# Kernel optimization log

Measured on AMD Instinct MI355X. Metric: run time of the kernel, lower is better.

## Reference

```python
import jax, jax.numpy as jnp
import numpy as np

N_NODES = 50000
N_EDGES = 500000
D_FEAT = 128
HIDDEN = 128
EPS = 1e-8


def _lin_init(key, fan_in, fan_out):
    return jax.random.normal(key, (fan_in, fan_out), dtype=jnp.float32) / np.sqrt(fan_in)


def setup_inputs() -> dict:
    key = jax.random.key(0)
    ks = jax.random.split(key, 16)
    h = jax.random.normal(ks[0], (N_NODES, D_FEAT), dtype=jnp.float32)
    coord = jax.random.normal(ks[1], (N_NODES, 3), dtype=jnp.float32)
    vel = jax.random.normal(ks[2], (N_NODES, 3), dtype=jnp.float32)
    edge_index = jax.random.randint(ks[3], (2, N_EDGES), 0, N_NODES, dtype=jnp.int32)
    return {
        "h": h, "coord": coord, "vel": vel, "edge_index": edge_index,
        "W_e1": _lin_init(ks[4], 2 * D_FEAT + 1, HIDDEN), "b_e1": jnp.zeros((HIDDEN,), jnp.float32),
        "W_e2": _lin_init(ks[5], HIDDEN, D_FEAT), "b_e2": jnp.zeros((D_FEAT,), jnp.float32),
        "W_c1": _lin_init(ks[6], D_FEAT, HIDDEN), "b_c1": jnp.zeros((HIDDEN,), jnp.float32),
        "W_c2": _lin_init(ks[7], HIDDEN, 1), "b_c2": jnp.zeros((1,), jnp.float32),
        "W_v1": _lin_init(ks[8], D_FEAT, HIDDEN), "b_v1": jnp.zeros((HIDDEN,), jnp.float32),
        "W_v2": _lin_init(ks[9], HIDDEN, 1), "b_v2": jnp.zeros((1,), jnp.float32),
        "W_n1": _lin_init(ks[10], 2 * D_FEAT, HIDDEN), "b_n1": jnp.zeros((HIDDEN,), jnp.float32),
        "W_n2": _lin_init(ks[11], HIDDEN, D_FEAT), "b_n2": jnp.zeros((D_FEAT,), jnp.float32),
    }


def reference(h, coord, vel, edge_index,
              W_e1, b_e1, W_e2, b_e2,
              W_c1, b_c1, W_c2, b_c2,
              W_v1, b_v1, W_v2, b_v2,
              W_n1, b_n1, W_n2, b_n2):
    act = jax.nn.silu
    r, c = edge_index[0], edge_index[1]
    n = coord.shape[0]

    # coord2radial with normalize=True
    diff = coord[r] - coord[c]                      # [E, 3]
    rad = jnp.sum(diff * diff, axis=-1, keepdims=True)  # [E, 1]
    norm = jnp.sqrt(jax.lax.stop_gradient(rad)) + EPS
    diff = diff / norm

    # edge_op: Linear -> act -> Linear -> act
    edge_in = jnp.concatenate([h[r], h[c], rad], axis=1)  # [E, 2D+1]
    m_ij = act(act(edge_in @ W_e1 + b_e1) @ W_e2 + b_e2)  # [E, D]

    # coord_op: Linear -> act -> Linear (scalar weight per edge)
    weights = act(m_ij @ W_c1 + b_c1) @ W_c2 + b_c2       # [E, 1]
    coors_sum = jax.ops.segment_sum(diff * weights, r, num_segments=n)  # [N, 3]

    # vel_op: Linear -> act -> Linear (scalar per node)
    vel_weights = act(h @ W_v1 + b_v1) @ W_v2 + b_v2      # [N, 1]
    coord_out = coord + coors_sum + vel * vel_weights

    # node aggregation + node_op: Linear -> act -> Linear
    m_i = jax.ops.segment_sum(m_ij, r, num_segments=h.shape[0])  # [N, D]
    agg = jnp.concatenate([h, m_i], axis=1)               # [N, 2D]
    h_out = act(agg @ W_n1 + b_n1) @ W_n2 + b_n2          # [N, D]
    return (h_out, coord_out)
```

## Files before the change

kernel.cpp:

```cpp
#include <hip/hip_runtime.h>
#include <stdint.h>

#define NN 50000
#define NE 500000
#define BLK 256
#define NEB ((NE + 127) / 128)
#define SST 136

#define BARRIER() asm volatile("s_waitcnt lgkmcnt(0)\n\ts_barrier" ::: "memory")

typedef __attribute__((ext_vector_type(8))) short bf16x8;
typedef __attribute__((ext_vector_type(4))) float f32x4;

__device__ __forceinline__ float silu(float x) { return x / (1.0f + __expf(-x)); }
__device__ __forceinline__ float bf2f(unsigned short s) {
    union { unsigned int u; float f; } v; v.u = ((unsigned int)s) << 16; return v.f;
}
__device__ __forceinline__ unsigned short f2bf(float f) {
    union { float f; unsigned int u; } v; v.f = f;
    return (unsigned short)((v.u + 0x7fffu + ((v.u >> 16) & 1u)) >> 16);
}
__device__ __forceinline__ unsigned int pack2(float a, float b) {
    return (unsigned int)f2bf(a) | ((unsigned int)f2bf(b) << 16);
}
__device__ __forceinline__ bf16x8 packf8(const float* p) {
    float4 f0 = *(const float4*)p; float4 f1 = *(const float4*)(p + 4);
    union { bf16x8 v; unsigned int u[4]; } o;
    o.u[0] = pack2(f0.x, f0.y); o.u[1] = pack2(f0.z, f0.w);
    o.u[2] = pack2(f1.x, f1.y); o.u[3] = pack2(f1.z, f1.w);
    return o.v;
}

__global__ void prep_h(const float* __restrict__ h, unsigned short* __restrict__ hb) {
    int i = blockIdx.x * 256 + threadIdx.x;
    if (i < NN * 128 / 4) {
        float4 v = ((const float4*)h)[i];
        uint2 o; o.x = pack2(v.x, v.y); o.y = pack2(v.z, v.w);
        ((uint2*)hb)[i] = o;
    }
}

__global__ void prep_w(const float* __restrict__ We1, const float* __restrict__ We2,
                       const float* __restrict__ Wc1, const float* __restrict__ Wv1,
                       const float* __restrict__ Wn1, const float* __restrict__ Wn2,
                       unsigned short* __restrict__ Wt1, unsigned short* __restrict__ Wt2,
                       unsigned short* __restrict__ Wt3, unsigned short* __restrict__ Wv1t,
                       unsigned short* __restrict__ Wn1t, unsigned short* __restrict__ Wn2t) {
    int i = blockIdx.x * 256 + threadIdx.x;
    if (i < 32768) {
        int j = i >> 8, k = i & 255;
        Wt1[i] = f2bf(We1[k * 128 + j]);
    } else if (i < 49152) {
        int t = i - 32768; int j = t >> 7, ks = t & 127;
        int k0 = (ks & 7) * 16 + (ks >> 3);
        Wt2[t] = f2bf(We2[k0 * 128 + j]);
    } else if (i < 65536) {
        int t = i - 49152; int j = t >> 7, ks = t & 127;
        int k0 = (ks & 7) * 16 + (ks >> 3);
        Wt3[t] = f2bf(Wc1[k0 * 128 + j]);
    } else if (i < 81920) {
        int t = i - 65536; int j = t >> 7, k = t & 127;
        Wv1t[t] = f2bf(Wv1[k * 128 + j]);
    } else if (i < 114688) {
        int t = i - 81920; int j = t >> 8, k = t & 255;
        int ksrc;
        if (k < 128) ksrc = k;
        else { int ks = k - 128; ksrc = 128 + (ks & 7) * 16 + (ks >> 3); }
        Wn1t[t] = f2bf(Wn1[ksrc * 128 + j]);
    } else if (i < 131072) {
        int t = i - 114688; int j = t >> 7, ks = t & 127;
        int k0 = (ks & 7) * 16 + (ks >> 3);
        Wn2t[t] = f2bf(Wn2[k0 * 128 + j]);
    }
}

__global__ void csr_count(const int* __restrict__ eidx, int* __restrict__ deg) {
    int e = blockIdx.x * 256 + threadIdx.x;
    if (e < NE) atomicAdd(&deg[eidx[e]], 1);
}

__global__ void scan_a(const int* __restrict__ deg, int* __restrict__ bsum) {
    __shared__ int s[256];
    int t = threadIdx.x, idx = blockIdx.x * 256 + t;
    s[t] = (idx < NN) ? deg[idx] : 0;
    __syncthreads();
    for (int off = 128; off > 0; off >>= 1) {
        if (t < off) s[t] += s[t + off];
        __syncthreads();
    }
    if (t == 0) bsum[blockIdx.x] = s[0];
}

__global__ void scan_b(int* __restrict__ bsum) {
    __shared__ int s[256];
    int t = threadIdx.x;
    int v = (t < 196) ? bsum[t] : 0;
    s[t] = v;
    __syncthreads();
    for (int off = 1; off < 256; off <<= 1) {
        int x = (t >= off) ? s[t - off] : 0;
        __syncthreads();
        s[t] += x;
        __syncthreads();
    }
    if (t < 196) bsum[t] = s[t] - v;
}

__global__ void scan_c(const int* __restrict__ deg, const int* __restrict__ bsum,
                       int* __restrict__ rowptr) {
    __shared__ int s[256];
    int t = threadIdx.x, idx = blockIdx.x * 256 + t;
    int v = (idx < NN) ? deg[idx] : 0;
    s[t] = v;
    __syncthreads();
    for (int off = 1; off < 256; off <<= 1) {
        int x = (t >= off) ? s[t - off] : 0;
        __syncthreads();
        s[t] += x;
        __syncthreads();
    }
    if (idx < NN) rowptr[idx] = bsum[blockIdx.x] + s[t] - v;
    if (idx == 0) rowptr[NN] = NE;
}

__global__ void csr_fill(const int* __restrict__ eidx, const int* __restrict__ rowptr,
                         int* __restrict__ cursor,
                         int* __restrict__ csr_r, int* __restrict__ csr_c) {
    int e = blockIdx.x * 256 + threadIdx.x;
    if (e < NE) {
        int r = eidx[e], c = eidx[NE + e];
        int slot = rowptr[r] + atomicAdd(&cursor[r], 1);
        csr_r[slot] = r; csr_c[slot] = c;
    }
}

__device__ __forceinline__ void stage256(const unsigned short* __restrict__ W, int halfk,
                                         unsigned short* sW, int tid) {
#pragma unroll
    for (int t = 0; t < 8; ++t) {
        int idx = tid + t * 256; int j = idx >> 4, g = idx & 15;
        *(uint4*)(sW + j * SST + g * 8) = *(const uint4*)(W + (size_t)j * 256 + halfk * 128 + g * 8);
    }
}
__device__ __forceinline__ void stage128(const unsigned short* __restrict__ W,
                                         unsigned short* sW, int tid) {
#pragma unroll
    for (int t = 0; t < 8; ++t) {
        int idx = tid + t * 256; int j = idx >> 4, g = idx & 15;
        *(uint4*)(sW + j * SST + g * 8) = *(const uint4*)(W + (size_t)j * 128 + g * 8);
    }
}
__device__ __forceinline__ void mfma4(const bf16x8 a[2][4], const unsigned short* sW,
                                      int l16, int q, f32x4 acc[2][8]) {
#pragma unroll
    for (int kc = 0; kc < 4; ++kc)
#pragma unroll
        for (int ct = 0; ct < 8; ++ct) {
            bf16x8 b = *(const bf16x8*)(sW + (ct * 16 + l16) * SST + kc * 32 + q * 8);
            acc[0][ct] = __builtin_amdgcn_mfma_f32_16x16x32_bf16(a[0][kc], b, acc[0][ct], 0, 0, 0);
            acc[1][ct] = __builtin_amdgcn_mfma_f32_16x16x32_bf16(a[1][kc], b, acc[1][ct], 0, 0, 0);
        }
}

__global__ __launch_bounds__(BLK, 2) void egcl_edge(
    const float* __restrict__ coord,
    const int* __restrict__ csr_r, const int* __restrict__ csr_c,
    const unsigned short* __restrict__ hb,
    const unsigned short* __restrict__ Wt1,
    const unsigned short* __restrict__ Wt2,
    const unsigned short* __restrict__ Wt3,
    const float* __restrict__ We1,
    const float* __restrict__ be1, const float* __restrict__ be2,
    const float* __restrict__ bc1,
    const float* __restrict__ Wc2, const float* __restrict__ bc2,
    float* __restrict__ m_acc, float* __restrict__ c_sum)
{
    __shared__ __align__(16) unsigned short sAb[128 * SST];
    __shared__ __align__(16) unsigned short sW[128 * SST];
    __shared__ float sRad[128], sDif[128][3];
    __shared__ int sRr[128], sRc[128], sSeg[128];
    __shared__ float sBe1[128], sBe2[128], sBc1[128], sWlast[128], sWc2f[128];

    const int tid = threadIdx.x;
    const int wv = tid >> 6, lane = tid & 63, q = lane >> 4, l16 = lane & 15;
    const int e0 = blockIdx.x * 128;

    if (tid < 128) {
        sBe1[tid] = be1[tid]; sBe2[tid] = be2[tid]; sBc1[tid] = bc1[tid];
        sWlast[tid] = We1[256 * 128 + tid]; sWc2f[tid] = Wc2[tid];
        int s = e0 + tid; int sc = (s < NE) ? s : (NE - 1);
        int r = csr_r[sc], c = csr_c[sc];
        sRr[tid] = r; sRc[tid] = c;
        sSeg[tid] = (s < NE) ? r : -1;
        float dx = coord[r * 3 + 0] - coord[c * 3 + 0];
        float dy = coord[r * 3 + 1] - coord[c * 3 + 1];
        float dz = coord[r * 3 + 2] - coord[c * 3 + 2];
        float rad = fmaf(dx, dx, fmaf(dy, dy, dz * dz));
        float inv = 1.0f / (sqrtf(rad) + 1e-8f);
        sRad[tid] = rad;
        sDif[tid][0] = dx * inv; sDif[tid][1] = dy * inv; sDif[tid][2] = dz * inv;
    }
    stage256(Wt1, 0, sW, tid);
    const float bc2v = bc2[0];
    BARRIER();

    f32x4 acc[2][8];
#pragma unroll
    for (int si = 0; si < 2; ++si)
#pragma unroll
        for (int ct = 0; ct < 8; ++ct) acc[si][ct] = (f32x4){0.f, 0.f, 0.f, 0.f};

    {
        bf16x8 a[2][4];
#pragma unroll
        for (int si = 0; si < 2; ++si) {
            int node = sRr[(wv * 2 + si) * 16 + l16];
#pragma unroll
            for (int kc = 0; kc < 4; ++kc)
                a[si][kc] = *(const bf16x8*)(hb + (size_t)node * 128 + kc * 32 + q * 8);
        }
        mfma4(a, sW, l16, q, acc);
    }
    BARRIER();
    stage256(Wt1, 1, sW, tid);
    BARRIER();
    {
        bf16x8 a[2][4];
#pragma unroll
        for (int si = 0; si < 2; ++si) {
            int node = sRc[(wv * 2 + si) * 16 + l16];
#pragma unroll
            for (int kc = 0; kc < 4; ++kc)
                a[si][kc] = *(const bf16x8*)(hb + (size_t)node * 128 + kc * 32 + q * 8);
        }
        mfma4(a, sW, l16, q, acc);
    }
    BARRIER();

#pragma unroll
    for (int si = 0; si < 2; ++si)
#pragma unroll
        for (int r = 0; r < 4; ++r) {
            int row = (wv * 2 + si) * 16 + q * 4 + r;
            float rad = sRad[row];
            float v[8];
#pragma unroll
            for (int ct = 0; ct < 8; ++ct) {
                int col = ct * 16 + l16;
                v[ct] = silu(acc[si][ct][r] + rad * sWlast[col] + sBe1[col]);
            }
            uint4 pk = make_uint4(pack2(v[0], v[1]), pack2(v[2], v[3]),
                                  pack2(v[4], v[5]), pack2(v[6], v[7]));
            *(uint4*)(sAb + row * SST + l16 * 8) = pk;
        }
    stage128(Wt2, sW, tid);
    BARRIER();

#pragma unroll
    for (int si = 0; si < 2; ++si)
#pragma unroll
        for (int ct = 0; ct < 8; ++ct) acc[si][ct] = (f32x4){0.f, 0.f, 0.f, 0.f};
    {
        bf16x8 a[2][4];
#pragma unroll
        for (int si = 0; si < 2; ++si) {
            int row = (wv * 2 + si) * 16 + l16;
#pragma unroll
            for (int kc = 0; kc < 4; ++kc)
                a[si][kc] = *(const bf16x8*)(sAb + row * SST + kc * 32 + q * 8);
        }
        mfma4(a, sW, l16, q, acc);
    }
    uint4 mu[2][4];
#pragma unroll
    for (int si = 0; si < 2; ++si)
#pragma unroll
        for (int r = 0; r < 4; ++r) {
            float v[8];
#pragma unroll
            for (int ct = 0; ct < 8; ++ct) v[ct] = silu(acc[si][ct][r] + sBe2[ct * 16 + l16]);
            mu[si][r] = make_uint4(pack2(v[0], v[1]), pack2(v[2], v[3]),
                                   pack2(v[4], v[5]), pack2(v[6], v[7]));
        }
    BARRIER();
#pragma unroll
    for (int si = 0; si < 2; ++si)
#pragma unroll
        for (int r = 0; r < 4; ++r) {
            int row = (wv * 2 + si) * 16 + q * 4 + r;
            *(uint4*)(sAb + row * SST + l16 * 8) = mu[si][r];
        }
    stage128(Wt3, sW, tid);
    BARRIER();

#pragma unroll
    for (int si = 0; si < 2; ++si)
#pragma unroll
        for (int ct = 0; ct < 8; ++ct) acc[si][ct] = (f32x4){0.f, 0.f, 0.f, 0.f};
    {
        bf16x8 a[2][4];
#pragma unroll
        for (int si = 0; si < 2; ++si) {
            int row = (wv * 2 + si) * 16 + l16;
#pragma unroll
            for (int kc = 0; kc < 4; ++kc)
                a[si][kc] = *(const bf16x8*)(sAb + row * SST + kc * 32 + q * 8);
        }
        mfma4(a, sW, l16, q, acc);
    }
#pragma unroll
    for (int si = 0; si < 2; ++si) {
        float p[4];
#pragma unroll
        for (int r = 0; r < 4; ++r) {
            float s = 0.f;
#pragma unroll
            for (int ct = 0; ct < 8; ++ct) {
                int col = ct * 16 + l16;
                float t = silu(acc[si][ct][r] + sBc1[col]);
                s = fmaf(t, sWc2f[col], s);
            }
            p[r] = s;
        }
#pragma unroll
        for (int m = 1; m < 16; m <<= 1)
#pragma unroll
            for (int r = 0; r < 4; ++r) p[r] += __shfl_xor(p[r], m, 16);
        if (l16 == 0) {
#pragma unroll
            for (int r = 0; r < 4; ++r) {
                int row = (wv * 2 + si) * 16 + q * 4 + r;
                int rn = sSeg[row];
                if (rn >= 0) {
                    float w = p[r] + bc2v;
                    atomicAdd(&c_sum[(size_t)rn * 3 + 0], sDif[row][0] * w);
                    atomicAdd(&c_sum[(size_t)rn * 3 + 1], sDif[row][1] * w);
                    atomicAdd(&c_sum[(size_t)rn * 3 + 2], sDif[row][2] * w);
                }
            }
        }
    }

    {
        int p = tid & 127, half = tid >> 7;
        int base = half * 64;
        float run = 0.f;
        int cur = sSeg[base];
        bool openL = true;
#pragma unroll 1
        for (int i = 0; i < 64; ++i) {
            int row = base + i;
            int rr = sSeg[row];
            if (rr != cur) {
                if (cur >= 0) {
                    float* dst = &m_acc[(size_t)cur * 128 + p];
                    if (openL) atomicAdd(dst, run);
                    else       *dst = run;
                }
                run = 0.f; cur = rr; openL = false;
            }
            run += bf2f(sAb[row * SST + p]);
        }
        if (cur >= 0) atomicAdd(&m_acc[(size_t)cur * 128 + p], run);
    }
}

__global__ __launch_bounds__(BLK, 3) void egcl_node(
    const unsigned short* __restrict__ hb,
    const float* __restrict__ coord,
    const float* __restrict__ vel,
    const unsigned short* __restrict__ Wv1t, const float* __restrict__ bv1,
    const float* __restrict__ Wv2, const float* __restrict__ bv2,
    const unsigned short* __restrict__ Wn1t, const float* __restrict__ bn1,
    const unsigned short* __restrict__ Wn2t, const float* __restrict__ bn2,
    const float* __restrict__ m_acc, const float* __restrict__ c_sum,
    float* __restrict__ out_h, float* __restrict__ out_c)
{
    __shared__ __align__(16) unsigned short sAb[128 * SST];
    __shared__ float sBv1[128], sWv2f[128], sBn1[128], sBn2[128];

    const int tid = threadIdx.x;
    const int wv = tid >> 6, lane = tid & 63, q = lane >> 4, l16 = lane & 15;
    const int n0 = blockIdx.x * 128;
    int nval = NN - n0; if (nval > 128) nval = 128;

    if (tid < 128) {
        sBv1[tid] = bv1[tid]; sWv2f[tid] = Wv2[tid];
        sBn1[tid] = bn1[tid]; sBn2[tid] = bn2[tid];
    }
    const float bv2v = bv2[0];

    bf16x8 ah[2][4], am[2][4];
#pragma unroll
    for (int si = 0; si < 2; ++si) {
        int row = (wv * 2 + si) * 16 + l16;
        int nn = n0 + row; if (nn >= NN) nn = NN - 1;
#pragma unroll
        for (int kc = 0; kc < 4; ++kc) {
            ah[si][kc] = *(const bf16x8*)(hb + (size_t)nn * 128 + kc * 32 + q * 8);
            am[si][kc] = packf8(m_acc + (size_t)nn * 128 + kc * 32 + q * 8);
        }
    }

    BARRIER();

    f32x4 acc[2][8];
#pragma unroll
    for (int si = 0; si < 2; ++si)
#pragma unroll
        for (int ct = 0; ct < 8; ++ct) acc[si][ct] = (f32x4){0.f, 0.f, 0.f, 0.f};
#pragma unroll
    for (int kc = 0; kc < 4; ++kc)
#pragma unroll
        for (int ct = 0; ct < 8; ++ct) {
            bf16x8 b = *(const bf16x8*)(Wv1t + (size_t)(ct * 16 + l16) * 128 + kc * 32 + q * 8);
            acc[0][ct] = __builtin_amdgcn_mfma_f32_16x16x32_bf16(ah[0][kc], b, acc[0][ct], 0, 0, 0);
            acc[1][ct] = __builtin_amdgcn_mfma_f32_16x16x32_bf16(ah[1][kc], b, acc[1][ct], 0, 0, 0);
        }
#pragma unroll
    for (int si = 0; si < 2; ++si) {
        float p[4];
#pragma unroll
        for (int r = 0; r < 4; ++r) {
            float s = 0.f;
#pragma unroll
            for (int ct = 0; ct < 8; ++ct) {
                int col = ct * 16 + l16;
                float t = silu(acc[si][ct][r] + sBv1[col]);
                s = fmaf(t, sWv2f[col], s);
            }
            p[r] = s;
        }
#pragma unroll
        for (int m = 1; m < 16; m <<= 1)
#pragma unroll
            for (int r = 0; r < 4; ++r) p[r] += __shfl_xor(p[r], m, 16);
        if (l16 == 0) {
#pragma unroll
            for (int r = 0; r < 4; ++r) {
                int row = (wv * 2 + si) * 16 + q * 4 + r;
                int n = n0 + row;
                if (row < nval) {
                    float vw = p[r] + bv2v;
#pragma unroll
                    for (int d = 0; d < 3; ++d) {
                        float cv = coord[(size_t)n * 3 + d] + c_sum[(size_t)n * 3 + d]
                                 + vel[(size_t)n * 3 + d] * vw;
                        out_c[(size_t)n * 3 + d] = cv;
                    }
                }
            }
        }
    }

#pragma unroll
    for (int si = 0; si < 2; ++si)
#pragma unroll
        for (int ct = 0; ct < 8; ++ct) acc[si][ct] = (f32x4){0.f, 0.f, 0.f, 0.f};
#pragma unroll
    for (int kc = 0; kc < 8; ++kc)
#pragma unroll
        for (int ct = 0; ct < 8; ++ct) {
            bf16x8 b = *(const bf16x8*)(Wn1t + (size_t)(ct * 16 + l16) * 256 + kc * 32 + q * 8);
            bf16x8 a0 = (kc < 4) ? ah[0][kc & 3] : am[0][kc & 3];
            bf16x8 a1 = (kc < 4) ? ah[1][kc & 3] : am[1][kc & 3];
            acc[0][ct] = __builtin_amdgcn_mfma_f32_16x16x32_bf16(a0, b, acc[0][ct], 0, 0, 0);
            acc[1][ct] = __builtin_amdgcn_mfma_f32_16x16x32_bf16(a1, b, acc[1][ct], 0, 0, 0);
        }
#pragma unroll
    for (int si = 0; si < 2; ++si)
#pragma unroll
        for (int r = 0; r < 4; ++r) {
            int row = (wv * 2 + si) * 16 + q * 4 + r;
            float v[8];
#pragma unroll
            for (int ct = 0; ct < 8; ++ct) v[ct] = silu(acc[si][ct][r] + sBn1[ct * 16 + l16]);
            uint4 pk = make_uint4(pack2(v[0], v[1]), pack2(v[2], v[3]),
                                  pack2(v[4], v[5]), pack2(v[6], v[7]));
            *(uint4*)(sAb + row * SST + l16 * 8) = pk;
        }

    BARRIER();

#pragma unroll
    for (int si = 0; si < 2; ++si)
#pragma unroll
        for (int ct = 0; ct < 8; ++ct) acc[si][ct] = (f32x4){0.f, 0.f, 0.f, 0.f};
    {
        bf16x8 a[2][4];
#pragma unroll
        for (int si = 0; si < 2; ++si) {
            int row = (wv * 2 + si) * 16 + l16;
#pragma unroll
            for (int kc = 0; kc < 4; ++kc)
                a[si][kc] = *(const bf16x8*)(sAb + row * SST + kc * 32 + q * 8);
        }
#pragma unroll
        for (int kc = 0; kc < 4; ++kc)
#pragma unroll
            for (int ct = 0; ct < 8; ++ct) {
                bf16x8 b = *(const bf16x8*)(Wn2t + (size_t)(ct * 16 + l16) * 128 + kc * 32 + q * 8);
                acc[0][ct] = __builtin_amdgcn_mfma_f32_16x16x32_bf16(a[0][kc], b, acc[0][ct], 0, 0, 0);
                acc[1][ct] = __builtin_amdgcn_mfma_f32_16x16x32_bf16(a[1][kc], b, acc[1][ct], 0, 0, 0);
            }
    }
#pragma unroll
    for (int si = 0; si < 2; ++si)
#pragma unroll
        for (int r = 0; r < 4; ++r) {
            int row = (wv * 2 + si) * 16 + q * 4 + r;
            if (row < nval) {
                float* orow = out_h + (size_t)(n0 + row) * 128;
#pragma unroll
                for (int ct = 0; ct < 8; ++ct)
                    orow[ct * 16 + l16] = acc[si][ct][r] + sBn2[ct * 16 + l16];
            }
        }
}

extern "C" void kernel_launch(void* const* d_in, const int* in_sizes, int n_in,
                              void* d_out, int out_size, void* d_ws, size_t ws_size,
                              hipStream_t stream) {
    const float* h     = (const float*)d_in[0];
    const float* coord = (const float*)d_in[1];
    const float* vel   = (const float*)d_in[2];
    const int*   eidx  = (const int*)d_in[3];
    const float* We1 = (const float*)d_in[4];
    const float* be1 = (const float*)d_in[5];
    const float* We2 = (const float*)d_in[6];
    const float* be2 = (const float*)d_in[7];
    const float* Wc1 = (const float*)d_in[8];
    const float* bc1 = (const float*)d_in[9];
    const float* Wc2 = (const float*)d_in[10];
    const float* bc2 = (const float*)d_in[11];
    const float* Wv1 = (const float*)d_in[12];
    const float* bv1 = (const float*)d_in[13];
    const float* Wv2 = (const float*)d_in[14];
    const float* bv2 = (const float*)d_in[15];
    const float* Wn1 = (const float*)d_in[16];
    const float* bn1 = (const float*)d_in[17];
    const float* Wn2 = (const float*)d_in[18];
    const float* bn2 = (const float*)d_in[19];

    char* ws = (char*)d_ws;
    float* m_acc = (float*)ws;
    float* c_sum = (float*)(ws + 25600000);
    unsigned short* hb   = (unsigned short*)(ws + 26200064);
    unsigned short* Wt1  = (unsigned short*)(ws + 39000064);
    unsigned short* Wt2  = (unsigned short*)(ws + 39065600);
    unsigned short* Wt3  = (unsigned short*)(ws + 39098368);
    unsigned short* Wv1t = (unsigned short*)(ws + 39131136);
    unsigned short* Wn1t = (unsigned short*)(ws + 39163904);
    unsigned short* Wn2t = (unsigned short*)(ws + 39229440);
    int* deg    = (int*)(ws + 39262208);
    int* cursor = (int*)(ws + 39462208);
    int* rowptr = (int*)(ws + 39662208);
    int* bsum   = (int*)(ws + 39862272);
    int* csr_r  = (int*)(ws + 39863296);
    int* csr_c  = (int*)(ws + 41863296);

    hipMemsetAsync(ws, 0, 26200000, stream);
    hipMemsetAsync(ws + 39262208, 0, 400000, stream);

    prep_h<<<6250, 256, 0, stream>>>(h, hb);
    prep_w<<<512, 256, 0, stream>>>(We1, We2, Wc1, Wv1, Wn1, Wn2,
                                    Wt1, Wt2, Wt3, Wv1t, Wn1t, Wn2t);

    csr_count<<<1954, 256, 0, stream>>>(eidx, deg);
    scan_a<<<196, 256, 0, stream>>>(deg, bsum);
    scan_b<<<1, 256, 0, stream>>>(bsum);
    scan_c<<<196, 256, 0, stream>>>(deg, bsum, rowptr);
    csr_fill<<<1954, 256, 0, stream>>>(eidx, rowptr, cursor, csr_r, csr_c);

    egcl_edge<<<NEB, BLK, 0, stream>>>(
        coord, csr_r, csr_c, hb, Wt1, Wt2, Wt3,
        We1, be1, be2, bc1, Wc2, bc2, m_acc, c_sum);

    float* out_h = (float*)d_out;
    float* out_c = out_h + (size_t)NN * 128;
    egcl_node<<<(NN + 127) / 128, BLK, 0, stream>>>(
        hb, coord, vel, Wv1t, bv1, Wv2, bv2, Wn1t, bn1, Wn2t, bn2,
        m_acc, c_sum, out_h, out_c);
}
```

Baseline: 459.7 us.

## Read edge weights from global memory, shrink LDS and node tiles, raise occupancy

The edge kernel no longer stages its weight matrices into shared memory. Each MFMA B-fragment is now read directly from global (L2-cached) bf16 weights, which removes the weight LDS buffer, the staging copies and several barriers, and the launch bound is raised to four blocks per CU. The node kernel now handles 64 nodes per block instead of 128, with one 16-row tile per wave and a smaller LDS buffer, again targeting higher occupancy. The workspace is reordered so the two zeroing memsets become one. In exchange, every wave issues redundant global and L2 weight loads, and per-wave MFMA work in the node kernel is halved.

```diff
diff --git a/kernel.cpp b/kernel.cpp
--- a/kernel.cpp
+++ b/kernel.cpp
@@ -134,35 +134,7 @@
     }
 }
 
-__device__ __forceinline__ void stage256(const unsigned short* __restrict__ W, int halfk,
-                                         unsigned short* sW, int tid) {
-#pragma unroll
-    for (int t = 0; t < 8; ++t) {
-        int idx = tid + t * 256; int j = idx >> 4, g = idx & 15;
-        *(uint4*)(sW + j * SST + g * 8) = *(const uint4*)(W + (size_t)j * 256 + halfk * 128 + g * 8);
-    }
-}
-__device__ __forceinline__ void stage128(const unsigned short* __restrict__ W,
-                                         unsigned short* sW, int tid) {
-#pragma unroll
-    for (int t = 0; t < 8; ++t) {
-        int idx = tid + t * 256; int j = idx >> 4, g = idx & 15;
-        *(uint4*)(sW + j * SST + g * 8) = *(const uint4*)(W + (size_t)j * 128 + g * 8);
-    }
-}
-__device__ __forceinline__ void mfma4(const bf16x8 a[2][4], const unsigned short* sW,
-                                      int l16, int q, f32x4 acc[2][8]) {
-#pragma unroll
-    for (int kc = 0; kc < 4; ++kc)
-#pragma unroll
-        for (int ct = 0; ct < 8; ++ct) {
-            bf16x8 b = *(const bf16x8*)(sW + (ct * 16 + l16) * SST + kc * 32 + q * 8);
-            acc[0][ct] = __builtin_amdgcn_mfma_f32_16x16x32_bf16(a[0][kc], b, acc[0][ct], 0, 0, 0);
-            acc[1][ct] = __builtin_amdgcn_mfma_f32_16x16x32_bf16(a[1][kc], b, acc[1][ct], 0, 0, 0);
-        }
-}
-
-__global__ __launch_bounds__(BLK, 2) void egcl_edge(
+__global__ __launch_bounds__(BLK, 4) void egcl_edge(
     const float* __restrict__ coord,
     const int* __restrict__ csr_r, const int* __restrict__ csr_c,
     const unsigned short* __restrict__ hb,
@@ -176,9 +148,8 @@
     float* __restrict__ m_acc, float* __restrict__ c_sum)
 {
     __shared__ __align__(16) unsigned short sAb[128 * SST];
-    __shared__ __align__(16) unsigned short sW[128 * SST];
     __shared__ float sRad[128], sDif[128][3];
-    __shared__ int sRr[128], sRc[128], sSeg[128];
+    __shared__ int sSeg[128];
     __shared__ float sBe1[128], sBe2[128], sBc1[128], sWlast[128], sWc2f[128];
 
     const int tid = threadIdx.x;
@@ -190,7 +161,6 @@
         sWlast[tid] = We1[256 * 128 + tid]; sWc2f[tid] = Wc2[tid];
         int s = e0 + tid; int sc = (s < NE) ? s : (NE - 1);
         int r = csr_r[sc], c = csr_c[sc];
-        sRr[tid] = r; sRc[tid] = c;
         sSeg[tid] = (s < NE) ? r : -1;
         float dx = coord[r * 3 + 0] - coord[c * 3 + 0];
         float dy = coord[r * 3 + 1] - coord[c * 3 + 1];
@@ -200,9 +170,7 @@
         sRad[tid] = rad;
         sDif[tid][0] = dx * inv; sDif[tid][1] = dy * inv; sDif[tid][2] = dz * inv;
     }
-    stage256(Wt1, 0, sW, tid);
     const float bc2v = bc2[0];
-    BARRIER();
 
     f32x4 acc[2][8];
 #pragma unroll
@@ -214,27 +182,41 @@
         bf16x8 a[2][4];
 #pragma unroll
         for (int si = 0; si < 2; ++si) {
-            int node = sRr[(wv * 2 + si) * 16 + l16];
+            int e = e0 + (wv * 2 + si) * 16 + l16; if (e >= NE) e = NE - 1;
+            int nr = csr_r[e];
 #pragma unroll
             for (int kc = 0; kc < 4; ++kc)
-                a[si][kc] = *(const bf16x8*)(hb + (size_t)node * 128 + kc * 32 + q * 8);
-        }
-        mfma4(a, sW, l16, q, acc);
-    }
-    BARRIER();
-    stage256(Wt1, 1, sW, tid);
-    BARRIER();
+                a[si][kc] = *(const bf16x8*)(hb + (size_t)nr * 128 + kc * 32 + q * 8);
+        }
+#pragma unroll
+        for (int kc = 0; kc < 4; ++kc)
+#pragma unroll
+            for (int ct = 0; ct < 8; ++ct) {
+                bf16x8 b = *(const bf16x8*)(Wt1 + (size_t)(ct * 16 + l16) * 256 + kc * 32 + q * 8);
+                acc[0][ct] = __builtin_amdgcn_mfma_f32_16x16x32_bf16(a[0][kc], b, acc[0][ct], 0, 0, 0);
+                acc[1][ct] = __builtin_amdgcn_mfma_f32_16x16x32_bf16(a[1][kc], b, acc[1][ct], 0, 0, 0);
+            }
+    }
     {
         bf16x8 a[2][4];
 #pragma unroll
         for (int si = 0; si < 2; ++si) {
-            int node = sRc[(wv * 2 + si) * 16 + l16];
+            int e = e0 + (wv * 2 + si) * 16 + l16; if (e >= NE) e = NE - 1;
+            int nc = csr_c[e];
 #pragma unroll
             for (int kc = 0; kc < 4; ++kc)
-                a[si][kc] = *(const bf16x8*)(hb + (size_t)node * 128 + kc * 32 + q * 8);
-        }
-        mfma4(a, sW, l16, q, acc);
-    }
+                a[si][kc] = *(const bf16x8*)(hb + (size_t)nc * 128 + kc * 32 + q * 8);
+        }
+#pragma unroll
+        for (int kc = 0; kc < 4; ++kc)
+#pragma unroll
+            for (int ct = 0; ct < 8; ++ct) {
+                bf16x8 b = *(const bf16x8*)(Wt1 + (size_t)(ct * 16 + l16) * 256 + 128 + kc * 32 + q * 8);
+                acc[0][ct] = __builtin_amdgcn_mfma_f32_16x16x32_bf16(a[0][kc], b, acc[0][ct], 0, 0, 0);
+                acc[1][ct] = __builtin_amdgcn_mfma_f32_16x16x32_bf16(a[1][kc], b, acc[1][ct], 0, 0, 0);
+            }
+    }
+
     BARRIER();
 
 #pragma unroll
@@ -253,7 +235,7 @@
                                   pack2(v[4], v[5]), pack2(v[6], v[7]));
             *(uint4*)(sAb + row * SST + l16 * 8) = pk;
         }
-    stage128(Wt2, sW, tid);
+
     BARRIER();
 
 #pragma unroll
@@ -269,7 +251,14 @@
             for (int kc = 0; kc < 4; ++kc)
                 a[si][kc] = *(const bf16x8*)(sAb + row * SST + kc * 32 + q * 8);
         }
-        mfma4(a, sW, l16, q, acc);
+#pragma unroll
+        for (int kc = 0; kc < 4; ++kc)
+#pragma unroll
+            for (int ct = 0; ct < 8; ++ct) {
+                bf16x8 b = *(const bf16x8*)(Wt2 + (size_t)(ct * 16 + l16) * 128 + kc * 32 + q * 8);
+                acc[0][ct] = __builtin_amdgcn_mfma_f32_16x16x32_bf16(a[0][kc], b, acc[0][ct], 0, 0, 0);
+                acc[1][ct] = __builtin_amdgcn_mfma_f32_16x16x32_bf16(a[1][kc], b, acc[1][ct], 0, 0, 0);
+            }
     }
     uint4 mu[2][4];
 #pragma unroll
@@ -290,7 +279,6 @@
             int row = (wv * 2 + si) * 16 + q * 4 + r;
             *(uint4*)(sAb + row * SST + l16 * 8) = mu[si][r];
         }
-    stage128(Wt3, sW, tid);
     BARRIER();
 
 #pragma unroll
@@ -306,7 +294,14 @@
             for (int kc = 0; kc < 4; ++kc)
                 a[si][kc] = *(const bf16x8*)(sAb + row * SST + kc * 32 + q * 8);
         }
-        mfma4(a, sW, l16, q, acc);
+#pragma unroll
+        for (int kc = 0; kc < 4; ++kc)
+#pragma unroll
+            for (int ct = 0; ct < 8; ++ct) {
+                bf16x8 b = *(const bf16x8*)(Wt3 + (size_t)(ct * 16 + l16) * 128 + kc * 32 + q * 8);
+                acc[0][ct] = __builtin_amdgcn_mfma_f32_16x16x32_bf16(a[0][kc], b, acc[0][ct], 0, 0, 0);
+                acc[1][ct] = __builtin_amdgcn_mfma_f32_16x16x32_bf16(a[1][kc], b, acc[1][ct], 0, 0, 0);
+            }
     }
 #pragma unroll
     for (int si = 0; si < 2; ++si) {
@@ -365,7 +360,7 @@
     }
 }
 
-__global__ __launch_bounds__(BLK, 3) void egcl_node(
+__global__ __launch_bounds__(BLK, 4) void egcl_node(
     const unsigned short* __restrict__ hb,
     const float* __restrict__ coord,
     const float* __restrict__ vel,
@@ -376,13 +371,13 @@
     const float* __restrict__ m_acc, const float* __restrict__ c_sum,
     float* __restrict__ out_h, float* __restrict__ out_c)
 {
-    __shared__ __align__(16) unsigned short sAb[128 * SST];
+    __shared__ __align__(16) unsigned short sAb[64 * SST];
     __shared__ float sBv1[128], sWv2f[128], sBn1[128], sBn2[128];
 
     const int tid = threadIdx.x;
     const int wv = tid >> 6, lane = tid & 63, q = lane >> 4, l16 = lane & 15;
-    const int n0 = blockIdx.x * 128;
-    int nval = NN - n0; if (nval > 128) nval = 128;
+    const int n0 = blockIdx.x * 64;
+    int nval = NN - n0; if (nval > 64) nval = 64;
 
     if (tid < 128) {
         sBv1[tid] = bv1[tid]; sWv2f[tid] = Wv2[tid];
@@ -390,35 +385,30 @@
     }
     const float bv2v = bv2[0];
 
-    bf16x8 ah[2][4], am[2][4];
-#pragma unroll
-    for (int si = 0; si < 2; ++si) {
-        int row = (wv * 2 + si) * 16 + l16;
+    bf16x8 ah[4], am[4];
+    {
+        int row = wv * 16 + l16;
         int nn = n0 + row; if (nn >= NN) nn = NN - 1;
 #pragma unroll
         for (int kc = 0; kc < 4; ++kc) {
-            ah[si][kc] = *(const bf16x8*)(hb + (size_t)nn * 128 + kc * 32 + q * 8);
-            am[si][kc] = packf8(m_acc + (size_t)nn * 128 + kc * 32 + q * 8);
+            ah[kc] = *(const bf16x8*)(hb + (size_t)nn * 128 + kc * 32 + q * 8);
+            am[kc] = packf8(m_acc + (size_t)nn * 128 + kc * 32 + q * 8);
         }
     }
 
     BARRIER();
 
-    f32x4 acc[2][8];
-#pragma unroll
-    for (int si = 0; si < 2; ++si)
-#pragma unroll
-        for (int ct = 0; ct < 8; ++ct) acc[si][ct] = (f32x4){0.f, 0.f, 0.f, 0.f};
+    f32x4 acc[8];
+#pragma unroll
+    for (int ct = 0; ct < 8; ++ct) acc[ct] = (f32x4){0.f, 0.f, 0.f, 0.f};
 #pragma unroll
     for (int kc = 0; kc < 4; ++kc)
 #pragma unroll
         for (int ct = 0; ct < 8; ++ct) {
             bf16x8 b = *(const bf16x8*)(Wv1t + (size_t)(ct * 16 + l16) * 128 + kc * 32 + q * 8);
-            acc[0][ct] = __builtin_amdgcn_mfma_f32_16x16x32_bf16(ah[0][kc], b, acc[0][ct], 0, 0, 0);
-            acc[1][ct] = __builtin_amdgcn_mfma_f32_16x16x32_bf16(ah[1][kc], b, acc[1][ct], 0, 0, 0);
-        }
-#pragma unroll
-    for (int si = 0; si < 2; ++si) {
+            acc[ct] = __builtin_amdgcn_mfma_f32_16x16x32_bf16(ah[kc], b, acc[ct], 0, 0, 0);
+        }
+    {
         float p[4];
 #pragma unroll
         for (int r = 0; r < 4; ++r) {
@@ -426,7 +416,7 @@
 #pragma unroll
             for (int ct = 0; ct < 8; ++ct) {
                 int col = ct * 16 + l16;
-                float t = silu(acc[si][ct][r] + sBv1[col]);
+                float t = silu(acc[ct][r] + sBv1[col]);
                 s = fmaf(t, sWv2f[col], s);
             }
             p[r] = s;
@@ -438,7 +428,7 @@
         if (l16 == 0) {
 #pragma unroll
             for (int r = 0; r < 4; ++r) {
-                int row = (wv * 2 + si) * 16 + q * 4 + r;
+                int row = wv * 16 + q * 4 + r;
                 int n = n0 + row;
                 if (row < nval) {
                     float vw = p[r] + bv2v;
@@ -454,68 +444,54 @@
     }
 
 #pragma unroll
-    for (int si = 0; si < 2; ++si)
-#pragma unroll
-        for (int ct = 0; ct < 8; ++ct) acc[si][ct] = (f32x4){0.f, 0.f, 0.f, 0.f};
+    for (int ct = 0; ct < 8; ++ct) acc[ct] = (f32x4){0.f, 0.f, 0.f, 0.f};
 #pragma unroll
     for (int kc = 0; kc < 8; ++kc)
 #pragma unroll
         for (int ct = 0; ct < 8; ++ct) {
             bf16x8 b = *(const bf16x8*)(Wn1t + (size_t)(ct * 16 + l16) * 256 + kc * 32 + q * 8);
-            bf16x8 a0 = (kc < 4) ? ah[0][kc & 3] : am[0][kc & 3];
-            bf16x8 a1 = (kc < 4) ? ah[1][kc & 3] : am[1][kc & 3];
-            acc[0][ct] = __builtin_amdgcn_mfma_f32_16x16x32_bf16(a0, b, acc[0][ct], 0, 0, 0);
-            acc[1][ct] = __builtin_amdgcn_mfma_f32_16x16x32_bf16(a1, b, acc[1][ct], 0, 0, 0);
-        }
-#pragma unroll
-    for (int si = 0; si < 2; ++si)
-#pragma unroll
-        for (int r = 0; r < 4; ++r) {
-            int row = (wv * 2 + si) * 16 + q * 4 + r;
-            float v[8];
-#pragma unroll
-            for (int ct = 0; ct < 8; ++ct) v[ct] = silu(acc[si][ct][r] + sBn1[ct * 16 + l16]);
-            uint4 pk = make_uint4(pack2(v[0], v[1]), pack2(v[2], v[3]),
-                                  pack2(v[4], v[5]), pack2(v[6], v[7]));
-            *(uint4*)(sAb + row * SST + l16 * 8) = pk;
-        }
+            bf16x8 a = (kc < 4) ? ah[kc & 3] : am[kc & 3];
+            acc[ct] = __builtin_amdgcn_mfma_f32_16x16x32_bf16(a, b, acc[ct], 0, 0, 0);
+        }
+#pragma unroll
+    for (int r = 0; r < 4; ++r) {
+        int row = wv * 16 + q * 4 + r;
+        float v[8];
+#pragma unroll
+        for (int ct = 0; ct < 8; ++ct) v[ct] = silu(acc[ct][r] + sBn1[ct * 16 + l16]);
+        uint4 pk = make_uint4(pack2(v[0], v[1]), pack2(v[2], v[3]),
+                              pack2(v[4], v[5]), pack2(v[6], v[7]));
+        *(uint4*)(sAb + row * SST + l16 * 8) = pk;
+    }
 
     BARRIER();
 
 #pragma unroll
-    for (int si = 0; si < 2; ++si)
-#pragma unroll
-        for (int ct = 0; ct < 8; ++ct) acc[si][ct] = (f32x4){0.f, 0.f, 0.f, 0.f};
-    {
-        bf16x8 a[2][4];
-#pragma unroll
-        for (int si = 0; si < 2; ++si) {
-            int row = (wv * 2 + si) * 16 + l16;
-#pragma unroll
-            for (int kc = 0; kc < 4; ++kc)
-                a[si][kc] = *(const bf16x8*)(sAb + row * SST + kc * 32 + q * 8);
-        }
+    for (int ct = 0; ct < 8; ++ct) acc[ct] = (f32x4){0.f, 0.f, 0.f, 0.f};
+    {
+        bf16x8 a[4];
+        int row = wv * 16 + l16;
 #pragma unroll
         for (int kc = 0; kc < 4; ++kc)
+            a[kc] = *(const bf16x8*)(sAb + row * SST + kc * 32 + q * 8);
+#pragma unroll
+        for (int kc = 0; kc < 4; ++kc)
 #pragma unroll
             for (int ct = 0; ct < 8; ++ct) {
                 bf16x8 b = *(const bf16x8*)(Wn2t + (size_t)(ct * 16 + l16) * 128 + kc * 32 + q * 8);
-                acc[0][ct] = __builtin_amdgcn_mfma_f32_16x16x32_bf16(a[0][kc], b, acc[0][ct], 0, 0, 0);
-                acc[1][ct] = __builtin_amdgcn_mfma_f32_16x16x32_bf16(a[1][kc], b, acc[1][ct], 0, 0, 0);
-            }
-    }
-#pragma unroll
-    for (int si = 0; si < 2; ++si)
-#pragma unroll
-        for (int r = 0; r < 4; ++r) {
-            int row = (wv * 2 + si) * 16 + q * 4 + r;
-            if (row < nval) {
-                float* orow = out_h + (size_t)(n0 + row) * 128;
-#pragma unroll
-                for (int ct = 0; ct < 8; ++ct)
-                    orow[ct * 16 + l16] = acc[si][ct][r] + sBn2[ct * 16 + l16];
-            }
-        }
+                acc[ct] = __builtin_amdgcn_mfma_f32_16x16x32_bf16(a[kc], b, acc[ct], 0, 0, 0);
+            }
+    }
+#pragma unroll
+    for (int r = 0; r < 4; ++r) {
+        int row = wv * 16 + q * 4 + r;
+        if (row < nval) {
+            float* orow = out_h + (size_t)(n0 + row) * 128;
+#pragma unroll
+            for (int ct = 0; ct < 8; ++ct)
+                orow[ct * 16 + l16] = acc[ct][r] + sBn2[ct * 16 + l16];
+        }
+    }
 }
 
 extern "C" void kernel_launch(void* const* d_in, const int* in_sizes, int n_in,
@@ -545,22 +521,21 @@
     char* ws = (char*)d_ws;
     float* m_acc = (float*)ws;
     float* c_sum = (float*)(ws + 25600000);
-    unsigned short* hb   = (unsigned short*)(ws + 26200064);
-    unsigned short* Wt1  = (unsigned short*)(ws + 39000064);
-    unsigned short* Wt2  = (unsigned short*)(ws + 39065600);
-    unsigned short* Wt3  = (unsigned short*)(ws + 39098368);
-    unsigned short* Wv1t = (unsigned short*)(ws + 39131136);
-    unsigned short* Wn1t = (unsigned short*)(ws + 39163904);
-    unsigned short* Wn2t = (unsigned short*)(ws + 39229440);
-    int* deg    = (int*)(ws + 39262208);
-    int* cursor = (int*)(ws + 39462208);
-    int* rowptr = (int*)(ws + 39662208);
-    int* bsum   = (int*)(ws + 39862272);
+    int* deg    = (int*)(ws + 26200000);
+    int* cursor = (int*)(ws + 26400000);
+    unsigned short* hb   = (unsigned short*)(ws + 26600000);
+    unsigned short* Wt1  = (unsigned short*)(ws + 39400000);
+    unsigned short* Wt2  = (unsigned short*)(ws + 39465536);
+    unsigned short* Wt3  = (unsigned short*)(ws + 39498304);
+    unsigned short* Wv1t = (unsigned short*)(ws + 39531072);
+    unsigned short* Wn1t = (unsigned short*)(ws + 39563840);
+    unsigned short* Wn2t = (unsigned short*)(ws + 39629376);
+    int* rowptr = (int*)(ws + 39662144);
+    int* bsum   = (int*)(ws + 39862208);
     int* csr_r  = (int*)(ws + 39863296);
     int* csr_c  = (int*)(ws + 41863296);
 
-    hipMemsetAsync(ws, 0, 26200000, stream);
-    hipMemsetAsync(ws + 39262208, 0, 400000, stream);
+    hipMemsetAsync(ws, 0, 26600000, stream);
 
     prep_h<<<6250, 256, 0, stream>>>(h, hb);
     prep_w<<<512, 256, 0, stream>>>(We1, We2, Wc1, Wv1, Wn1, Wn2,
@@ -578,7 +553,7 @@
 
     float* out_h = (float*)d_out;
     float* out_c = out_h + (size_t)NN * 128;
-    egcl_node<<<(NN + 127) / 128, BLK, 0, stream>>>(
+    egcl_node<<<(NN + 63) / 64, BLK, 0, stream>>>(
         hb, coord, vel, Wv1t, bv1, Wv2, bv2, Wn1t, bn1, Wn2t, bn2,
         m_acc, c_sum, out_h, out_c);
 }
```

New measurement: 582.5 us. 1.27x slower.
